# Kernel optimization log

Measured on AMD Instinct MI355X. Metric: run time of the kernel, lower is better.

## Reference

```python
import jax, jax.numpy as jnp
import numpy as np

NUM_HEADS = 12
HEAD_DIM = 64  # d_out // num_heads = 768 // 12


def setup_inputs() -> dict:
    key = jax.random.key(0)
    k1, k2 = jax.random.split(key)
    x = jax.random.normal(k1, (2, 2048, 768), dtype=jnp.float32)
    # torch Linear weight: [d_out, d_in], y = x @ W.T
    Wq = jax.random.normal(k2, (768, 768), dtype=jnp.float32) * 0.02
    return {"x": x, "Wq": Wq}


def reference(x, Wq):
    b, n, d_in = x.shape
    H, hd = NUM_HEADS, HEAD_DIM
    d_out = H * hd
    # NOTE: the original module uses Wq for queries, keys AND values.
    qkv = x @ Wq.T                                   # [b, n, d_out]
    h = qkv.reshape(b, n, H, hd).transpose(0, 2, 1, 3)  # [b, H, n, hd]
    scores = jnp.einsum('bhqd,bhkd->bhqk', h, h)      # [b, H, n, n]
    causal = jnp.triu(jnp.ones((n, n), dtype=bool), k=1)
    scores = jnp.where(causal, -jnp.inf, scores)
    attn = jax.nn.softmax(scores / jnp.sqrt(jnp.float32(hd)), axis=-1)
    ctx = jnp.einsum('bhqk,bhkd->bhqd', attn, h)      # [b, H, n, hd]
    # faithful to source: transpose(-2,-1) -> [b, H, hd, n], then view(b, n, d_out)
    ctx = ctx.transpose(0, 1, 3, 2)
    return ctx.reshape(b, n, d_out)
```

## Files before the change

### kernel.cpp

```cpp
#include <hip/hip_runtime.h>
#include <math.h>

typedef __attribute__((ext_vector_type(8))) short  short8;
typedef __attribute__((ext_vector_type(4))) float  floatx4;
typedef __attribute__((ext_vector_type(4))) unsigned short ushort4v;

#define MFMA16(a, b, c) __builtin_amdgcn_mfma_f32_16x16x32_bf16(a, b, c, 0, 0, 0)

constexpr int NSEQ = 2048;
constexpr int DIN  = 768;
constexpr int NH   = 12;
constexpr size_t NX = (size_t)2 * NSEQ * DIN;
constexpr size_t NW = (size_t)DIN * DIN;
constexpr float QSCALE = 0.18033688011112042f;

__device__ __forceinline__ ushort f2bf(float f) {
    unsigned u = __float_as_uint(f);
    u += 0x7FFF + ((u >> 16) & 1);
    return (ushort)(u >> 16);
}
__device__ __forceinline__ float bf2f(ushort u) {
    return __uint_as_float(((unsigned)u) << 16);
}

__global__ __launch_bounds__(256)
void cvt_bf16(const float* __restrict__ x, const float* __restrict__ Wq,
              ushort* __restrict__ dst)
{
    size_t i = ((size_t)blockIdx.x * 256 + threadIdx.x) * 8;
    const float* s = (i < NX) ? (x + i) : (Wq + (i - NX));
    float4 f0 = ((const float4*)s)[0];
    float4 f1 = ((const float4*)s)[1];
    short8 o;
    o[0] = (short)f2bf(f0.x); o[1] = (short)f2bf(f0.y);
    o[2] = (short)f2bf(f0.z); o[3] = (short)f2bf(f0.w);
    o[4] = (short)f2bf(f1.x); o[5] = (short)f2bf(f1.y);
    o[6] = (short)f2bf(f1.z); o[7] = (short)f2bf(f1.w);
    *(short8*)(dst + i) = o;
}

__global__ __launch_bounds__(256, 3)
void qkv_mfma(const ushort* __restrict__ xb, const ushort* __restrict__ wb,
              ushort* __restrict__ h)
{
    __shared__ ushort As[64 * 72];
    __shared__ ushort Bs[128 * 72];

    const int tid  = threadIdx.x;
    const int w    = tid >> 6;
    const int lane = tid & 63;
    const int m    = lane & 15;
    const int quad = lane >> 4;
    const int r0   = blockIdx.x * 64;
    const int c0   = blockIdx.y * 128;
    const int mrow0 = (w & 1) * 32;
    const int ncol0 = (w >> 1) * 64;

    floatx4 C[2][4] = {};
    short8 ar[2], br[4];

    #pragma unroll
    for (int i = 0; i < 2; ++i) {
        int id = tid + i * 256;
        ar[i] = *(const short8*)(xb + (size_t)(r0 + (id >> 3)) * DIN + (id & 7) * 8);
    }
    #pragma unroll
    for (int i = 0; i < 4; ++i) {
        int id = tid + i * 256;
        br[i] = *(const short8*)(wb + (size_t)(c0 + (id >> 3)) * DIN + (id & 7) * 8);
    }

    for (int kk = 0; kk < 12; ++kk) {
        __syncthreads();
        #pragma unroll
        for (int i = 0; i < 2; ++i) {
            int id = tid + i * 256;
            *(short8*)&As[(id >> 3) * 72 + (id & 7) * 8] = ar[i];
        }
        #pragma unroll
        for (int i = 0; i < 4; ++i) {
            int id = tid + i * 256;
            *(short8*)&Bs[(id >> 3) * 72 + (id & 7) * 8] = br[i];
        }
        if (kk < 11) {
            const int k0 = (kk + 1) * 64;
            #pragma unroll
            for (int i = 0; i < 2; ++i) {
                int id = tid + i * 256;
                ar[i] = *(const short8*)(xb + (size_t)(r0 + (id >> 3)) * DIN + k0 + (id & 7) * 8);
            }
            #pragma unroll
            for (int i = 0; i < 4; ++i) {
                int id = tid + i * 256;
                br[i] = *(const short8*)(wb + (size_t)(c0 + (id >> 3)) * DIN + k0 + (id & 7) * 8);
            }
        }
        __syncthreads();

        #pragma unroll
        for (int kt2 = 0; kt2 < 2; ++kt2) {
            short8 a0 = *(const short8*)&As[(mrow0 + m)      * 72 + kt2 * 32 + quad * 8];
            short8 a1 = *(const short8*)&As[(mrow0 + 16 + m) * 72 + kt2 * 32 + quad * 8];
            #pragma unroll
            for (int nt = 0; nt < 4; ++nt) {
                short8 bf = *(const short8*)&Bs[(ncol0 + nt * 16 + m) * 72 + kt2 * 32 + quad * 8];
                C[0][nt] = MFMA16(a0, bf, C[0][nt]);
                C[1][nt] = MFMA16(a1, bf, C[1][nt]);
            }
        }
    }

    #pragma unroll
    for (int mt = 0; mt < 2; ++mt)
        #pragma unroll
        for (int nt = 0; nt < 4; ++nt) {
            int cg = c0 + ncol0 + nt * 16 + m;
            int head = cg >> 6, d = cg & 63;
            #pragma unroll
            for (int r = 0; r < 4; ++r) {
                int rg = r0 + mrow0 + mt * 16 + quad * 4 + r;
                int b = rg >> 11, q = rg & 2047;
                h[((size_t)(b * NH + head) * NSEQ + q) * 64 + d] = f2bf(C[mt][nt][r]);
            }
        }
}

__global__ __launch_bounds__(256, 4)
void attn_mfma(const ushort* __restrict__ h, float* __restrict__ out)
{
    __shared__ ushort Ks[64 * 72];
    __shared__ ushort Vt[64 * 72];
    __shared__ ushort Ps[4 * 16 * 72];

    const int tid  = threadIdx.x;
    const int w    = tid >> 6;
    const int lane = tid & 63;
    const int m    = lane & 15;
    const int quad = lane >> 4;

    const int qt = 31 - blockIdx.x;
    const int bh = blockIdx.y;
    const int q0 = qt * 64;
    const int wq = q0 + w * 16;
    const ushort* __restrict__ Hh = h + (size_t)bh * NSEQ * 64;

    short8 qa[2];
    #pragma unroll
    for (int kt2 = 0; kt2 < 2; ++kt2) {
        short8 raw = *(const short8*)(Hh + (size_t)(wq + m) * 64 + kt2 * 32 + quad * 8);
        #pragma unroll
        for (int j = 0; j < 8; ++j)
            qa[kt2][j] = (short)f2bf(bf2f((ushort)raw[j]) * QSCALE);
    }

    floatx4 O[4] = {};
    float lacc = 0.0f;
    ushort* Psw = Ps + w * 16 * 72;

    const int kr2  = (tid & 31) * 2;
    const int part = tid >> 5;
    const int nkt  = qt + 1;

    short8 a0, a1;
    {
        const ushort* src = Hh + (size_t)kr2 * 64 + part * 8;
        a0 = *(const short8*)src;
        a1 = *(const short8*)(src + 64);
    }

    for (int kt = 0; kt < nkt; ++kt) {
        __syncthreads();
        union { short8 v; ushort u[8]; } ua, ub;
        ua.v = a0; ub.v = a1;
        *(short8*)&Ks[kr2       * 72 + part * 8] = a0;
        *(short8*)&Ks[(kr2 + 1) * 72 + part * 8] = a1;
        #pragma unroll
        for (int i = 0; i < 8; ++i) {
            unsigned pk = (unsigned)ua.u[i] | ((unsigned)ub.u[i] << 16);
            *(unsigned*)&Vt[(part * 8 + i) * 72 + kr2] = pk;
        }
        if (kt + 1 < nkt) {
            const ushort* src = Hh + (size_t)((kt + 1) * 64 + kr2) * 64 + part * 8;
            a0 = *(const short8*)src;
            a1 = *(const short8*)(src + 64);
        }
        __syncthreads();

        floatx4 S[4] = {};
        #pragma unroll
        for (int kt2 = 0; kt2 < 2; ++kt2)
            #pragma unroll
            for (int mt = 0; mt < 4; ++mt) {
                short8 ka = *(const short8*)&Ks[(mt * 16 + m) * 72 + kt2 * 32 + quad * 8];
                S[mt] = MFMA16(ka, qa[kt2], S[mt]);
            }

        const int k0 = kt * 64;
        if (kt == nkt - 1) {
            #pragma unroll
            for (int mt = 0; mt < 4; ++mt) {
                ushort4v pw;
                #pragma unroll
                for (int r = 0; r < 4; ++r) {
                    int kg = k0 + mt * 16 + quad * 4 + r;
                    float p = (kg <= wq + m) ? exp2f(S[mt][r]) : 0.0f;
                    lacc += p;
                    pw[r] = f2bf(p);
                }
                *(ushort4v*)&Psw[m * 72 + mt * 16 + quad * 4] = pw;
            }
        } else {
            #pragma unroll
            for (int mt = 0; mt < 4; ++mt) {
                ushort4v pw;
                #pragma unroll
                for (int r = 0; r < 4; ++r) {
                    float p = exp2f(S[mt][r]);
                    lacc += p;
                    pw[r] = f2bf(p);
                }
                *(ushort4v*)&Psw[m * 72 + mt * 16 + quad * 4] = pw;
            }
        }

        #pragma unroll
        for (int kt2 = 0; kt2 < 2; ++kt2) {
            short8 pb = *(const short8*)&Psw[m * 72 + kt2 * 32 + quad * 8];
            #pragma unroll
            for (int mt = 0; mt < 4; ++mt) {
                short8 va = *(const short8*)&Vt[(mt * 16 + m) * 72 + kt2 * 32 + quad * 8];
                O[mt] = MFMA16(va, pb, O[mt]);
            }
        }
    }

    lacc += __shfl_xor(lacc, 16);
    lacc += __shfl_xor(lacc, 32);
    float linv = 1.0f / lacc;

    #pragma unroll
    for (int mt = 0; mt < 4; ++mt)
        #pragma unroll
        for (int r = 0; r < 4; ++r) {
            int d = mt * 16 + quad * 4 + r;
            out[((size_t)bh * 64 + d) * NSEQ + q0 + w * 16 + m] = O[mt][r] * linv;
        }
}

extern "C" void kernel_launch(void* const* d_in, const int* in_sizes, int n_in,
                              void* d_out, int out_size, void* d_ws, size_t ws_size,
                              hipStream_t stream)
{
    (void)in_sizes; (void)n_in; (void)out_size; (void)ws_size;
    const float* x  = (const float*)d_in[0];
    const float* Wq = (const float*)d_in[1];
    float* out = (float*)d_out;

    ushort* xb = (ushort*)d_ws;
    ushort* wb = xb + NX;
    ushort* hb = wb + NW;

    cvt_bf16<<<dim3((NX + NW) / (8 * 256)), dim3(256), 0, stream>>>(x, Wq, xb);
    qkv_mfma<<<dim3(64, 6), dim3(256), 0, stream>>>(xb, wb, hb);
    attn_mfma<<<dim3(32, 24), dim3(256), 0, stream>>>(hb, out);
}
```

Baseline: 131.3 us.

## Shrink GEMM and attention tiles for more blocks, add packed bf16 convert

```diff
diff --git a/kernel.cpp b/kernel.cpp
--- a/kernel.cpp
+++ b/kernel.cpp
@@ -3,7 +3,6 @@
 
 typedef __attribute__((ext_vector_type(8))) short  short8;
 typedef __attribute__((ext_vector_type(4))) float  floatx4;
-typedef __attribute__((ext_vector_type(4))) unsigned short ushort4v;
 
 #define MFMA16(a, b, c) __builtin_amdgcn_mfma_f32_16x16x32_bf16(a, b, c, 0, 0, 0)
 
@@ -21,6 +20,11 @@
 }
 __device__ __forceinline__ float bf2f(ushort u) {
     return __uint_as_float(((unsigned)u) << 16);
+}
+__device__ __forceinline__ unsigned cvt_pk_bf16(float lo, float hi) {
+    unsigned r;
+    asm("v_cvt_pk_bf16_f32 %0, %1, %2" : "=v"(r) : "v"(lo), "v"(hi));
+    return r;
 }
 
 __global__ __launch_bounds__(256)
@@ -44,7 +48,7 @@
               ushort* __restrict__ h)
 {
     __shared__ ushort As[64 * 72];
-    __shared__ ushort Bs[128 * 72];
+    __shared__ ushort Bs[64 * 72];
 
     const int tid  = threadIdx.x;
     const int w    = tid >> 6;
@@ -52,21 +56,17 @@
     const int m    = lane & 15;
     const int quad = lane >> 4;
     const int r0   = blockIdx.x * 64;
-    const int c0   = blockIdx.y * 128;
+    const int c0   = blockIdx.y * 64;
     const int mrow0 = (w & 1) * 32;
-    const int ncol0 = (w >> 1) * 64;
-
-    floatx4 C[2][4] = {};
-    short8 ar[2], br[4];
+    const int ncol0 = (w >> 1) * 32;
+
+    floatx4 C[2][2] = {};
+    short8 ar[2], br[2];
 
     #pragma unroll
     for (int i = 0; i < 2; ++i) {
         int id = tid + i * 256;
         ar[i] = *(const short8*)(xb + (size_t)(r0 + (id >> 3)) * DIN + (id & 7) * 8);
-    }
-    #pragma unroll
-    for (int i = 0; i < 4; ++i) {
-        int id = tid + i * 256;
         br[i] = *(const short8*)(wb + (size_t)(c0 + (id >> 3)) * DIN + (id & 7) * 8);
     }
 
@@ -76,10 +76,6 @@
         for (int i = 0; i < 2; ++i) {
             int id = tid + i * 256;
             *(short8*)&As[(id >> 3) * 72 + (id & 7) * 8] = ar[i];
-        }
-        #pragma unroll
-        for (int i = 0; i < 4; ++i) {
-            int id = tid + i * 256;
             *(short8*)&Bs[(id >> 3) * 72 + (id & 7) * 8] = br[i];
         }
         if (kk < 11) {
@@ -88,10 +84,6 @@
             for (int i = 0; i < 2; ++i) {
                 int id = tid + i * 256;
                 ar[i] = *(const short8*)(xb + (size_t)(r0 + (id >> 3)) * DIN + k0 + (id & 7) * 8);
-            }
-            #pragma unroll
-            for (int i = 0; i < 4; ++i) {
-                int id = tid + i * 256;
                 br[i] = *(const short8*)(wb + (size_t)(c0 + (id >> 3)) * DIN + k0 + (id & 7) * 8);
             }
         }
@@ -101,19 +93,19 @@
         for (int kt2 = 0; kt2 < 2; ++kt2) {
             short8 a0 = *(const short8*)&As[(mrow0 + m)      * 72 + kt2 * 32 + quad * 8];
             short8 a1 = *(const short8*)&As[(mrow0 + 16 + m) * 72 + kt2 * 32 + quad * 8];
-            #pragma unroll
-            for (int nt = 0; nt < 4; ++nt) {
-                short8 bf = *(const short8*)&Bs[(ncol0 + nt * 16 + m) * 72 + kt2 * 32 + quad * 8];
-                C[0][nt] = MFMA16(a0, bf, C[0][nt]);
-                C[1][nt] = MFMA16(a1, bf, C[1][nt]);
-            }
+            short8 b0 = *(const short8*)&Bs[(ncol0 + m)      * 72 + kt2 * 32 + quad * 8];
+            short8 b1 = *(const short8*)&Bs[(ncol0 + 16 + m) * 72 + kt2 * 32 + quad * 8];
+            C[0][0] = MFMA16(a0, b0, C[0][0]);
+            C[0][1] = MFMA16(a0, b1, C[0][1]);
+            C[1][0] = MFMA16(a1, b0, C[1][0]);
+            C[1][1] = MFMA16(a1, b1, C[1][1]);
         }
     }
 
     #pragma unroll
     for (int mt = 0; mt < 2; ++mt)
         #pragma unroll
-        for (int nt = 0; nt < 4; ++nt) {
+        for (int nt = 0; nt < 2; ++nt) {
             int cg = c0 + ncol0 + nt * 16 + m;
             int head = cg >> 6, d = cg & 63;
             #pragma unroll
@@ -125,12 +117,12 @@
         }
 }
 
-__global__ __launch_bounds__(256, 4)
+__global__ __launch_bounds__(128, 3)
 void attn_mfma(const ushort* __restrict__ h, float* __restrict__ out)
 {
     __shared__ ushort Ks[64 * 72];
     __shared__ ushort Vt[64 * 72];
-    __shared__ ushort Ps[4 * 16 * 72];
+    __shared__ ushort Ps[2 * 16 * 72];
 
     const int tid  = threadIdx.x;
     const int w    = tid >> 6;
@@ -138,10 +130,13 @@
     const int m    = lane & 15;
     const int quad = lane >> 4;
 
-    const int qt = 31 - blockIdx.x;
+    const int xi = blockIdx.x;
     const int bh = blockIdx.y;
-    const int q0 = qt * 64;
+    const int t  = bh >> 2;
+    const int qt = (t & 1) ? xi : (63 - xi);
+    const int q0 = qt * 32;
     const int wq = q0 + w * 16;
+    const int nkt = (qt >> 1) + 1;
     const ushort* __restrict__ Hh = h + (size_t)bh * NSEQ * 64;
 
     short8 qa[2];
@@ -159,30 +154,36 @@
 
     const int kr2  = (tid & 31) * 2;
     const int part = tid >> 5;
-    const int nkt  = qt + 1;
-
-    short8 a0, a1;
+    const int db   = part * 16;
+
+    short8 pre[4];
     {
-        const ushort* src = Hh + (size_t)kr2 * 64 + part * 8;
-        a0 = *(const short8*)src;
-        a1 = *(const short8*)(src + 64);
+        const ushort* src = Hh + (size_t)kr2 * 64 + db;
+        pre[0] = *(const short8*)src;
+        pre[1] = *(const short8*)(src + 8);
+        pre[2] = *(const short8*)(src + 64);
+        pre[3] = *(const short8*)(src + 72);
     }
 
     for (int kt = 0; kt < nkt; ++kt) {
         __syncthreads();
-        union { short8 v; ushort u[8]; } ua, ub;
-        ua.v = a0; ub.v = a1;
-        *(short8*)&Ks[kr2       * 72 + part * 8] = a0;
-        *(short8*)&Ks[(kr2 + 1) * 72 + part * 8] = a1;
+        *(short8*)&Ks[kr2       * 72 + db]     = pre[0];
+        *(short8*)&Ks[kr2       * 72 + db + 8] = pre[1];
+        *(short8*)&Ks[(kr2 + 1) * 72 + db]     = pre[2];
+        *(short8*)&Ks[(kr2 + 1) * 72 + db + 8] = pre[3];
+        union { short8 v; ushort u[8]; } a0, a1, b0, b1;
+        a0.v = pre[0]; a1.v = pre[1]; b0.v = pre[2]; b1.v = pre[3];
         #pragma unroll
         for (int i = 0; i < 8; ++i) {
-            unsigned pk = (unsigned)ua.u[i] | ((unsigned)ub.u[i] << 16);
-            *(unsigned*)&Vt[(part * 8 + i) * 72 + kr2] = pk;
+            *(unsigned*)&Vt[(db + i)     * 72 + kr2] = (unsigned)a0.u[i] | ((unsigned)b0.u[i] << 16);
+            *(unsigned*)&Vt[(db + 8 + i) * 72 + kr2] = (unsigned)a1.u[i] | ((unsigned)b1.u[i] << 16);
         }
         if (kt + 1 < nkt) {
-            const ushort* src = Hh + (size_t)((kt + 1) * 64 + kr2) * 64 + part * 8;
-            a0 = *(const short8*)src;
-            a1 = *(const short8*)(src + 64);
+            const ushort* src = Hh + (size_t)((kt + 1) * 64 + kr2) * 64 + db;
+            pre[0] = *(const short8*)src;
+            pre[1] = *(const short8*)(src + 8);
+            pre[2] = *(const short8*)(src + 64);
+            pre[3] = *(const short8*)(src + 72);
         }
         __syncthreads();
 
@@ -195,31 +196,32 @@
                 S[mt] = MFMA16(ka, qa[kt2], S[mt]);
             }
 
-        const int k0 = kt * 64;
+        const int lim = wq + m - kt * 64;
         if (kt == nkt - 1) {
             #pragma unroll
             for (int mt = 0; mt < 4; ++mt) {
-                ushort4v pw;
-                #pragma unroll
-                for (int r = 0; r < 4; ++r) {
-                    int kg = k0 + mt * 16 + quad * 4 + r;
-                    float p = (kg <= wq + m) ? exp2f(S[mt][r]) : 0.0f;
-                    lacc += p;
-                    pw[r] = f2bf(p);
-                }
-                *(ushort4v*)&Psw[m * 72 + mt * 16 + quad * 4] = pw;
+                float p0 = (mt * 16 + quad * 4 + 0 <= lim) ? exp2f(S[mt][0]) : 0.0f;
+                float p1 = (mt * 16 + quad * 4 + 1 <= lim) ? exp2f(S[mt][1]) : 0.0f;
+                float p2 = (mt * 16 + quad * 4 + 2 <= lim) ? exp2f(S[mt][2]) : 0.0f;
+                float p3 = (mt * 16 + quad * 4 + 3 <= lim) ? exp2f(S[mt][3]) : 0.0f;
+                lacc += (p0 + p1) + (p2 + p3);
+                uint2 pw;
+                pw.x = cvt_pk_bf16(p0, p1);
+                pw.y = cvt_pk_bf16(p2, p3);
+                *(uint2*)&Psw[m * 72 + mt * 16 + quad * 4] = pw;
             }
         } else {
             #pragma unroll
             for (int mt = 0; mt < 4; ++mt) {
-                ushort4v pw;
-                #pragma unroll
-                for (int r = 0; r < 4; ++r) {
-                    float p = exp2f(S[mt][r]);
-                    lacc += p;
-                    pw[r] = f2bf(p);
-                }
-                *(ushort4v*)&Psw[m * 72 + mt * 16 + quad * 4] = pw;
+                float p0 = exp2f(S[mt][0]);
+                float p1 = exp2f(S[mt][1]);
+                float p2 = exp2f(S[mt][2]);
+                float p3 = exp2f(S[mt][3]);
+                lacc += (p0 + p1) + (p2 + p3);
+                uint2 pw;
+                pw.x = cvt_pk_bf16(p0, p1);
+                pw.y = cvt_pk_bf16(p2, p3);
+                *(uint2*)&Psw[m * 72 + mt * 16 + quad * 4] = pw;
             }
         }
 
@@ -261,6 +263,6 @@
     ushort* hb = wb + NW;
 
     cvt_bf16<<<dim3((NX + NW) / (8 * 256)), dim3(256), 0, stream>>>(x, Wq, xb);
-    qkv_mfma<<<dim3(64, 6), dim3(256), 0, stream>>>(xb, wb, hb);
-    attn_mfma<<<dim3(32, 24), dim3(256), 0, stream>>>(hb, out);
-}
+    qkv_mfma<<<dim3(64, 12), dim3(256), 0, stream>>>(xb, wb, hb);
+    attn_mfma<<<dim3(64, 24), dim3(128), 0, stream>>>(hb, out);
+}
```

New measurement: 119.4 us. 1.1x faster.
